# Kernel tuning notes

Hardware: AMD Instinct MI355X
Metric: run time of the kernel (lower is better)

Reference implementation:

```python
import jax, jax.numpy as jnp
import numpy as np

SEQ_LEN = 64  # config.SEQ_LEN
T, B, N, D = 256, 128, 4, 2
H_HIS, H_INT = 32, 8


def _uniform(key, shape, k):
    return jax.random.uniform(key, shape, jnp.float32, -k, k)


def setup_inputs() -> dict:
    key = jax.random.key(0)
    ks = jax.random.split(key, 12)
    kh = 1.0 / np.sqrt(H_HIS)
    ki = 1.0 / np.sqrt(H_INT)
    ko = 1.0 / np.sqrt(40)
    return {
        "inputs": jax.random.normal(ks[0], (T, B, N, D), jnp.float32),
        # history LSTM (input 2 -> hidden 32), gate order i,f,g,o like torch
        "Wih_his": _uniform(ks[1], (4 * H_HIS, D), kh),
        "Whh_his": _uniform(ks[2], (4 * H_HIS, H_HIS), kh),
        "bih_his": _uniform(ks[3], (4 * H_HIS,), kh),
        "bhh_his": _uniform(ks[4], (4 * H_HIS,), kh),
        # interaction LSTM (input 2 -> hidden 8)
        "Wih_int": _uniform(ks[5], (4 * H_INT, D), ki),
        "Whh_int": _uniform(ks[6], (4 * H_INT, H_INT), ki),
        "bih_int": _uniform(ks[7], (4 * H_INT,), ki),
        "bhh_int": _uniform(ks[8], (4 * H_INT,), ki),
        # output Linear(40 -> 2)
        "W_out": _uniform(ks[9], (2, H_HIS + H_INT), ko),
        "b_out": _uniform(ks[10], (2,), ko),
    }


def _lstm_windows(x_w, valid, Wih, Whh, bih, bhh):
    """Run an LSTM over L steps for T independent windows at once.
    x_w: [L, Tw, B, d]  inputs per step (leading padding for short windows)
    valid: [L, Tw] bool; while False the state is held at zero, which is
    exactly equivalent to starting the window fresh at its first valid step.
    Returns final hidden state h: [Tw, B, H].
    """
    H = Whh.shape[1]
    Tw, Bb = x_w.shape[1], x_w.shape[2]
    b = bih + bhh

    def step(carry, xs):
        h, c = carry
        x, v = xs
        g = x @ Wih.T + h @ Whh.T + b            # [Tw, B, 4H]
        i, f, gg, o = jnp.split(g, 4, axis=-1)
        c_new = jax.nn.sigmoid(f) * c + jax.nn.sigmoid(i) * jnp.tanh(gg)
        h_new = jax.nn.sigmoid(o) * jnp.tanh(c_new)
        m = v[:, None, None]
        return (jnp.where(m, h_new, 0.0), jnp.where(m, c_new, 0.0)), None

    init = (jnp.zeros((Tw, Bb, H), x_w.dtype), jnp.zeros((Tw, Bb, H), x_w.dtype))
    (h, _), _ = jax.lax.scan(step, init, (x_w, valid))
    return h


def reference(inputs, Wih_his, Whh_his, bih_his, bhh_his,
              Wih_int, Whh_int, bih_int, bhh_int, W_out, b_out):
    Tt, Bb, Nn, Dd = inputs.shape
    L = SEQ_LEN
    # window index for output frame t: frames t-L+1 .. t (clipped; invalid masked)
    t = jnp.arange(Tt)[:, None]
    s = jnp.arange(L)[None, :]
    idx = t - (L - 1) + s                      # [T, L]
    valid = (idx >= 0)
    idx_c = jnp.clip(idx, 0, Tt - 1)
    x_his = inputs[:, :, -1, :][idx_c]         # [T, L, B, d] (ego / last node)
    x_int = inputs[:, :, 0, :][idx_c]          # [T, L, B, d] (interaction node)
    x_his = jnp.transpose(x_his, (1, 0, 2, 3))  # [L, T, B, d]
    x_int = jnp.transpose(x_int, (1, 0, 2, 3))
    v = jnp.transpose(valid)                   # [L, T]

    h_his = _lstm_windows(x_his, v, Wih_his, Whh_his, bih_his, bhh_his)  # [T,B,32]
    h_int = _lstm_windows(x_int, v, Wih_int, Whh_int, bih_int, bhh_int)  # [T,B,8]
    emb = jnp.concatenate([h_his, h_int], axis=-1)                       # [T,B,40]
    return emb @ W_out.T + b_out                                         # [T,B,2]
```

## Files before the change

kernel.cpp:

```cpp
#include <hip/hip_runtime.h>


typedef float v4f __attribute__((ext_vector_type(4)));
typedef _Float16 h8v __attribute__((ext_vector_type(8)));

static __device__ __forceinline__ float fexp2(float x) {
    return __builtin_amdgcn_exp2f(x);
}
static __device__ __forceinline__ float frcp(float x) {
    return __builtin_amdgcn_rcpf(x);
}
static __device__ __forceinline__ unsigned short f2h(float f) {
    _Float16 h = (_Float16)f;
    unsigned short u;
    __builtin_memcpy(&u, &h, 2);
    return u;
}
static __device__ __forceinline__ float h2f(unsigned short u) {
    _Float16 h;
    __builtin_memcpy(&h, &u, 2);
    return (float)h;
}

#define LOG2E    1.442695041f
#define TWOLOG2E 2.885390082f
#define H16ONE   0x3C00u

static __device__ __forceinline__ void lstm_unit(
    float Di, float Df, float Dg, float Do, float& c, float& h)
{
    const float ei = fminf(fexp2(Di), 1e12f);
    const float ef = fminf(fexp2(Df), 1e12f);
    const float eg = fminf(fexp2(Dg), 1e12f);
    const float eo = fminf(fexp2(Do), 1e18f);
    const float pi1 = 1.f + ei, pf1 = 1.f + ef, pg1 = 1.f + eg;
    const float p12 = pi1 * pg1;
    const float r3  = frcp(p12 * pf1);
    const float cn  = fmaf(p12, c, (1.f - eg) * pf1) * r3;
    c = cn;
    const float ec = fminf(fexp2(TWOLOG2E * cn), 1e18f);
    h = (ec - 1.f) * frcp((1.f + eo) * (1.f + ec));
}

__global__ __launch_bounds__(256) void prep_kernel(
    const float* __restrict__ Wih_his, const float* __restrict__ Whh_his,
    const float* __restrict__ bih_his, const float* __restrict__ bhh_his,
    const float* __restrict__ Wih_int, const float* __restrict__ Whh_int,
    const float* __restrict__ bih_int, const float* __restrict__ bhh_int,
    float* __restrict__ ws)
{
    const int i = blockIdx.x * 256 + threadIdx.x;
    unsigned short* wsu = reinterpret_cast<unsigned short*>(ws);

    if (i < 4096) {
        const int T8 = i >> 9, m = (i >> 5) & 15, k = i & 31;
        const int w = T8 >> 2, Tl = T8 & 3;
        const int orig = Tl * 32 + w * 16 + m;
        const float s = (Tl == 2) ? -TWOLOG2E : -LOG2E;
        wsu[i] = f2h(Whh_his[orig * 32 + k] * s);
    } else if (i < 8192) {
        const int e = i - 4096;
        const int T8 = e >> 9, m = (e >> 5) & 15, k = e & 31;
        const int w = T8 >> 2, Tl = T8 & 3;
        const int orig = Tl * 32 + w * 16 + m;
        const float s = (Tl == 2) ? -TWOLOG2E : -LOG2E;
        const float w0 = Wih_his[orig * 2] * s;
        const float w1 = Wih_his[orig * 2 + 1] * s;
        const float b  = (bih_his[orig] + bhh_his[orig]) * s;
        unsigned short v = 0;
        switch (k) {
            case 0: v = f2h(w0); break;
            case 1: v = f2h(w1); break;
            case 2: v = f2h(b);  break;
            case 3: v = f2h(w0 - h2f(f2h(w0))); break;
            case 4: v = f2h(w1 - h2f(f2h(w1))); break;
            case 5: v = f2h(b  - h2f(f2h(b)));  break;
            case 6: v = f2h(w0); break;
            case 7: v = f2h(w1); break;
            default: v = 0; break;
        }
        wsu[4096 + e] = v;
    } else if (i < 9216) {
        const int e = i - 8192;
        const int T = e >> 9, m = (e >> 5) & 15, k = e & 31;
        const int q = k >> 3, j = k & 7;
        const int g = 2 * T + ((m & 3) >> 1);
        const int u = 2 * (m >> 2) + (m & 1);
        const int orig = g * 8 + u;
        const float s = (g == 2) ? -TWOLOG2E : -LOG2E;
        unsigned short v = 0;
        if (j < 6) {
            const int col = 2 * q + (j & 1);
            const float w = Whh_int[orig * 8 + col] * s;
            v = (j == 2 || j == 3) ? f2h(w - h2f(f2h(w))) : f2h(w);
        } else {
            const int comp = j & 1;
            if (q <= 1) {
                v = f2h(Wih_int[orig * 2 + comp] * s);
            } else if (q == 2) {
                const float w = Wih_int[orig * 2 + comp] * s;
                v = f2h(w - h2f(f2h(w)));
            } else {
                const float b = (bih_int[orig] + bhh_int[orig]) * s;
                v = (comp == 0) ? f2h(b) : f2h(b - h2f(f2h(b)));
            }
        }
        wsu[8192 + e] = v;
    }
}

__global__ __launch_bounds__(128, 4) void fused2_kernel(
    const float* __restrict__ inp, const float* __restrict__ ws,
    const float* __restrict__ W_out, const float* __restrict__ b_out,
    float* __restrict__ out)
{
    __shared__ __align__(16) unsigned char hb[2][1280];
    __shared__ float2 ebuf[16];

    const int tid  = threadIdx.x;
    const int w    = tid >> 6;
    const int lane = tid & 63;
    const int n    = lane & 15;
    const int q    = lane >> 4;
    const int Wd   = blockIdx.x;
    const int t    = Wd >> 3;
    const int bg   = Wd & 7;
    const int nsteps = (t >= 63) ? 64 : (t + 1);
    const int tau0   = (t >= 63) ? (t - 63) : 0;

    const unsigned short* wsu = reinterpret_cast<const unsigned short*>(ws);
    const h8v* wa = reinterpret_cast<const h8v*>(wsu);
    const h8v* wx = reinterpret_cast<const h8v*>(wsu + 4096);
    const h8v* wi = reinterpret_cast<const h8v*>(wsu + 8192);
    h8v AW[4], AX[4], AI[2];
#pragma unroll
    for (int Tl = 0; Tl < 4; ++Tl) {
        AW[Tl] = wa[(w * 4 + Tl) * 64 + n * 4 + q];
        AX[Tl] = wx[(w * 4 + Tl) * 64 + n * 4 + q];
    }
#pragma unroll
    for (int T = 0; T < 2; ++T) AI[T] = wi[T * 64 + n * 4 + q];

    const int chain = bg * 16 + n;
    const float* xb0 = inp + chain * 8;
    float2 xvH = *reinterpret_cast<const float2*>(xb0 + tau0 * 1024 + 6);
    float2 xvI = *reinterpret_cast<const float2*>(xb0 + tau0 * 1024);

    union BU { unsigned u[4]; h8v h; };
    BU bh;  bh.u[0] = bh.u[1] = bh.u[2] = bh.u[3] = 0;
    BU bhI; bhI.u[0] = bhI.u[1] = bhI.u[2] = bhI.u[3] = 0;
    float cH[4] = {0.f, 0.f, 0.f, 0.f};
    float hH[4] = {0.f, 0.f, 0.f, 0.f};
    float cI0 = 0.f, cI1 = 0.f, ih0 = 0.f, ih1 = 0.f;

    const int wb = n * 80 + w * 32 + q * 8;
    const int rb = n * 80 + q * 16;

#pragma unroll 1
    for (int s = 0; s < nsteps; ++s) {
        const int sn = (s + 1 < nsteps) ? (s + 1) : (nsteps - 1);
        const float* xr = xb0 + (tau0 + sn) * 1024;
        const float2 xnH = *reinterpret_cast<const float2*>(xr + 6);
        const float2 xnI = *reinterpret_cast<const float2*>(xr);

        BU bx;
        {
            const unsigned short xh = f2h(xvH.x), yh = f2h(xvH.y);
            const unsigned short xl = f2h(xvH.x - h2f(xh));
            const unsigned short yl = f2h(xvH.y - h2f(yh));
            bx.u[0] = ((unsigned)yh << 16) | xh;
            bx.u[1] = ((unsigned)xh << 16) | H16ONE;
            bx.u[2] = (H16ONE << 16) | yh;
            bx.u[3] = ((unsigned)yl << 16) | xl;
            if (q != 0) { bx.u[0] = 0; bx.u[1] = 0; bx.u[2] = 0; bx.u[3] = 0; }
        }

        const v4f z = {0.f, 0.f, 0.f, 0.f};

        if (w == 1) {
            const unsigned short xh = f2h(xvI.x), yh = f2h(xvI.y);
            const unsigned short xl = f2h(xvI.x - h2f(xh));
            const unsigned short yl = f2h(xvI.y - h2f(yh));
            const unsigned ph = ((unsigned)yh << 16) | xh;
            const unsigned pl = ((unsigned)yl << 16) | xl;
            bhI.u[3] = (q == 3) ? ((H16ONE << 16) | H16ONE)
                                : ((q == 1) ? pl : ph);
            const v4f E0 = __builtin_amdgcn_mfma_f32_16x16x32_f16(AI[0], bhI.h, z, 0, 0, 0);
            const v4f E1 = __builtin_amdgcn_mfma_f32_16x16x32_f16(AI[1], bhI.h, z, 0, 0, 0);
            lstm_unit(E0[0], E0[2], E1[0], E1[2], cI0, ih0);
            lstm_unit(E0[1], E0[3], E1[1], E1[3], cI1, ih1);
            const unsigned short hh0 = f2h(ih0), hh1 = f2h(ih1);
            const unsigned short hl0 = f2h(ih0 - h2f(hh0));
            const unsigned short hl1 = f2h(ih1 - h2f(hh1));
            bhI.u[0] = ((unsigned)hh1 << 16) | hh0;
            bhI.u[1] = bhI.u[0];
            bhI.u[2] = ((unsigned)hl1 << 16) | hl0;
        }

        v4f D[4];
#pragma unroll
        for (int Tl = 0; Tl < 4; ++Tl) {
            const v4f cx = __builtin_amdgcn_mfma_f32_16x16x32_f16(AX[Tl], bx.h, z, 0, 0, 0);
            D[Tl] = __builtin_amdgcn_mfma_f32_16x16x32_f16(AW[Tl], bh.h, cx, 0, 0, 0);
        }

#pragma unroll
        for (int r = 0; r < 4; ++r)
            lstm_unit(D[0][r], D[1][r], D[2][r], D[3][r], cH[r], hH[r]);

        {
            const unsigned p0 = ((unsigned)f2h(hH[1]) << 16) | f2h(hH[0]);
            const unsigned p1 = ((unsigned)f2h(hH[3]) << 16) | f2h(hH[2]);
            *reinterpret_cast<uint2*>(&hb[s & 1][wb]) = make_uint2(p0, p1);
        }
        __syncthreads();
        {
            const uint4 rv = *reinterpret_cast<const uint4*>(&hb[s & 1][rb]);
            bh.u[0] = rv.x; bh.u[1] = rv.y; bh.u[2] = rv.z; bh.u[3] = rv.w;
        }

        xvH = xnH;
        xvI = xnI;
    }

    const int u0 = w * 16 + q * 4;
    float e0 = 0.f, e1 = 0.f;
#pragma unroll
    for (int r = 0; r < 4; ++r) {
        e0 = fmaf(W_out[u0 + r],      hH[r], e0);
        e1 = fmaf(W_out[40 + u0 + r], hH[r], e1);
    }
    if (w == 1) {
        e0 = fmaf(W_out[33 + 2 * q], ih1, fmaf(W_out[32 + 2 * q], ih0, e0));
        e1 = fmaf(W_out[73 + 2 * q], ih1, fmaf(W_out[72 + 2 * q], ih0, e1));
    }
    e0 += __shfl_xor(e0, 16); e1 += __shfl_xor(e1, 16);
    e0 += __shfl_xor(e0, 32); e1 += __shfl_xor(e1, 32);

    if (w == 1 && lane < 16) {
        float2 p; p.x = e0; p.y = e1;
        ebuf[n] = p;
    }
    __syncthreads();
    if (w == 0 && lane < 16) {
        const float2 p = ebuf[n];
        float2 o;
        o.x = e0 + p.x + b_out[0];
        o.y = e1 + p.y + b_out[1];
        reinterpret_cast<float2*>(out)[t * 128 + chain] = o;
    }
}

extern "C" void kernel_launch(void* const* d_in, const int* in_sizes, int n_in,
                              void* d_out, int out_size, void* d_ws, size_t ws_size,
                              hipStream_t stream) {
    const float* inp     = (const float*)d_in[0];
    const float* Wih_his = (const float*)d_in[1];
    const float* Whh_his = (const float*)d_in[2];
    const float* bih_his = (const float*)d_in[3];
    const float* bhh_his = (const float*)d_in[4];
    const float* Wih_int = (const float*)d_in[5];
    const float* Whh_int = (const float*)d_in[6];
    const float* bih_int = (const float*)d_in[7];
    const float* bhh_int = (const float*)d_in[8];
    const float* W_out   = (const float*)d_in[9];
    const float* b_out   = (const float*)d_in[10];
    float* out  = (float*)d_out;
    float* ws   = (float*)d_ws;

    prep_kernel<<<dim3(36), dim3(256), 0, stream>>>(
        Wih_his, Whh_his, bih_his, bhh_his,
        Wih_int, Whh_int, bih_int, bhh_int, ws);

    fused2_kernel<<<dim3(2048), dim3(128), 0, stream>>>(
        inp, ws, W_out, b_out, out);
}
```

Baseline: 177.0 us.

## Emit early-frame outputs from one shared prefix chain instead of separate windows

Result: no change. 179.4 us (+1.4%).

```diff
diff --git a/kernel.cpp b/kernel.cpp
--- a/kernel.cpp
+++ b/kernel.cpp
@@ -115,7 +115,7 @@
     float* __restrict__ out)
 {
     __shared__ __align__(16) unsigned char hb[2][1280];
-    __shared__ float2 ebuf[16];
+    __shared__ float2 ebuf[2][16];
 
     const int tid  = threadIdx.x;
     const int w    = tid >> 6;
@@ -123,10 +123,10 @@
     const int n    = lane & 15;
     const int q    = lane >> 4;
     const int Wd   = blockIdx.x;
-    const int t    = Wd >> 3;
+    const int j    = Wd >> 3;
     const int bg   = Wd & 7;
-    const int nsteps = (t >= 63) ? 64 : (t + 1);
-    const int tau0   = (t >= 63) ? (t - 63) : 0;
+    const int tau0 = j;
+    const bool readout = (j == 0);
 
     const unsigned short* wsu = reinterpret_cast<const unsigned short*>(ws);
     const h8v* wa = reinterpret_cast<const h8v*>(wsu);
@@ -157,8 +157,8 @@
     const int rb = n * 80 + q * 16;
 
 #pragma unroll 1
-    for (int s = 0; s < nsteps; ++s) {
-        const int sn = (s + 1 < nsteps) ? (s + 1) : (nsteps - 1);
+    for (int s = 0; s < 64; ++s) {
+        const int sn = (s < 63) ? (s + 1) : 63;
         const float* xr = xb0 + (tau0 + sn) * 1024;
         const float2 xnH = *reinterpret_cast<const float2*>(xr + 6);
         const float2 xnI = *reinterpret_cast<const float2*>(xr);
@@ -208,6 +208,26 @@
         for (int r = 0; r < 4; ++r)
             lstm_unit(D[0][r], D[1][r], D[2][r], D[3][r], cH[r], hH[r]);
 
+        float re0 = 0.f, re1 = 0.f;
+        if (readout) {
+            const int u0 = w * 16 + q * 4;
+#pragma unroll
+            for (int r = 0; r < 4; ++r) {
+                re0 = fmaf(W_out[u0 + r],      hH[r], re0);
+                re1 = fmaf(W_out[40 + u0 + r], hH[r], re1);
+            }
+            if (w == 1) {
+                re0 = fmaf(W_out[33 + 2 * q], ih1, fmaf(W_out[32 + 2 * q], ih0, re0));
+                re1 = fmaf(W_out[73 + 2 * q], ih1, fmaf(W_out[72 + 2 * q], ih0, re1));
+            }
+            re0 += __shfl_xor(re0, 16); re1 += __shfl_xor(re1, 16);
+            re0 += __shfl_xor(re0, 32); re1 += __shfl_xor(re1, 32);
+            if (w == 1 && lane < 16) {
+                float2 p; p.x = re0; p.y = re1;
+                ebuf[s & 1][n] = p;
+            }
+        }
+
         {
             const unsigned p0 = ((unsigned)f2h(hH[1]) << 16) | f2h(hH[0]);
             const unsigned p1 = ((unsigned)f2h(hH[3]) << 16) | f2h(hH[2]);
@@ -219,35 +239,45 @@
             bh.u[0] = rv.x; bh.u[1] = rv.y; bh.u[2] = rv.z; bh.u[3] = rv.w;
         }
 
+        if (readout && w == 0 && lane < 16) {
+            const float2 p = ebuf[s & 1][n];
+            float2 o;
+            o.x = re0 + p.x + b_out[0];
+            o.y = re1 + p.y + b_out[1];
+            reinterpret_cast<float2*>(out)[s * 128 + chain] = o;
+        }
+
         xvH = xnH;
         xvI = xnI;
     }
 
-    const int u0 = w * 16 + q * 4;
-    float e0 = 0.f, e1 = 0.f;
-#pragma unroll
-    for (int r = 0; r < 4; ++r) {
-        e0 = fmaf(W_out[u0 + r],      hH[r], e0);
-        e1 = fmaf(W_out[40 + u0 + r], hH[r], e1);
-    }
-    if (w == 1) {
-        e0 = fmaf(W_out[33 + 2 * q], ih1, fmaf(W_out[32 + 2 * q], ih0, e0));
-        e1 = fmaf(W_out[73 + 2 * q], ih1, fmaf(W_out[72 + 2 * q], ih0, e1));
-    }
-    e0 += __shfl_xor(e0, 16); e1 += __shfl_xor(e1, 16);
-    e0 += __shfl_xor(e0, 32); e1 += __shfl_xor(e1, 32);
-
-    if (w == 1 && lane < 16) {
-        float2 p; p.x = e0; p.y = e1;
-        ebuf[n] = p;
-    }
-    __syncthreads();
-    if (w == 0 && lane < 16) {
-        const float2 p = ebuf[n];
-        float2 o;
-        o.x = e0 + p.x + b_out[0];
-        o.y = e1 + p.y + b_out[1];
-        reinterpret_cast<float2*>(out)[t * 128 + chain] = o;
+    if (!readout) {
+        const int u0 = w * 16 + q * 4;
+        float e0 = 0.f, e1 = 0.f;
+#pragma unroll
+        for (int r = 0; r < 4; ++r) {
+            e0 = fmaf(W_out[u0 + r],      hH[r], e0);
+            e1 = fmaf(W_out[40 + u0 + r], hH[r], e1);
+        }
+        if (w == 1) {
+            e0 = fmaf(W_out[33 + 2 * q], ih1, fmaf(W_out[32 + 2 * q], ih0, e0));
+            e1 = fmaf(W_out[73 + 2 * q], ih1, fmaf(W_out[72 + 2 * q], ih0, e1));
+        }
+        e0 += __shfl_xor(e0, 16); e1 += __shfl_xor(e1, 16);
+        e0 += __shfl_xor(e0, 32); e1 += __shfl_xor(e1, 32);
+
+        if (w == 1 && lane < 16) {
+            float2 p; p.x = e0; p.y = e1;
+            ebuf[0][n] = p;
+        }
+        __syncthreads();
+        if (w == 0 && lane < 16) {
+            const float2 p = ebuf[0][n];
+            float2 o;
+            o.x = e0 + p.x + b_out[0];
+            o.y = e1 + p.y + b_out[1];
+            reinterpret_cast<float2*>(out)[(63 + j) * 128 + chain] = o;
+        }
     }
 }
 
@@ -272,6 +302,6 @@
         Wih_his, Whh_his, bih_his, bhh_his,
         Wih_int, Whh_int, bih_int, bhh_int, ws);
 
-    fused2_kernel<<<dim3(2048), dim3(128), 0, stream>>>(
+    fused2_kernel<<<dim3(1544), dim3(128), 0, stream>>>(
         inp, ws, W_out, b_out, out);
 }
```
